# Kernel tuning notes

Measured on AMD Instinct MI355X. Metric: run time of the kernel, lower is better.

The kernel has to match this reference:

```python
import jax, jax.numpy as jnp
import numpy as np
import math

EMBED_DIM = 768
NUM_HEADS = 12
HEAD_DIM = EMBED_DIM // NUM_HEADS
R = 16
LORA_ALPHA = 16
SCALING = LORA_ALPHA / math.sqrt(R)  # 4.0
U = 1.0  # ramp_up_steps=0 -> u()=1.0


def lora_linear(x, W, b, A):
    # base F.linear + SingLoRA delta: delta_W = A @ A.T (symmetric)
    base = x @ W.T + b
    delta_W = A @ A.T  # [D, D]
    return base + (x @ delta_W.T) * (U * SCALING)


def setup_inputs() -> dict:
    key = jax.random.key(0)
    ks = jax.random.split(key, 16)
    B, S, D = 2, 2048, EMBED_DIM
    inv = 1.0 / math.sqrt(D)
    d = {
        'query': jax.random.normal(ks[0], (B, S, D), jnp.float32),
        'key': jax.random.normal(ks[1], (B, S, D), jnp.float32),
        'value': jax.random.normal(ks[2], (B, S, D), jnp.float32),
        'Wq': jax.random.normal(ks[3], (D, D), jnp.float32) * inv,
        'bq': jax.random.normal(ks[4], (D,), jnp.float32) * 0.01,
        'Aq': jax.random.normal(ks[5], (D, R), jnp.float32) * 0.01,
        'Wk': jax.random.normal(ks[6], (D, D), jnp.float32) * inv,
        'bk': jax.random.normal(ks[7], (D,), jnp.float32) * 0.01,
        'Ak': jax.random.normal(ks[8], (D, R), jnp.float32) * 0.01,
        'Wv': jax.random.normal(ks[9], (D, D), jnp.float32) * inv,
        'bv': jax.random.normal(ks[10], (D,), jnp.float32) * 0.01,
        'Av': jax.random.normal(ks[11], (D, R), jnp.float32) * 0.01,
        'Wo': jax.random.normal(ks[12], (D, D), jnp.float32) * inv,
        'bo': jax.random.normal(ks[13], (D,), jnp.float32) * 0.01,
    }
    return d


def reference(query, key, value, Wq, bq, Aq, Wk, bk, Ak, Wv, bv, Av, Wo, bo):
    B, S, D = query.shape
    H, hd = NUM_HEADS, HEAD_DIM
    q = lora_linear(query, Wq, bq, Aq)
    k = lora_linear(key, Wk, bk, Ak)
    v = lora_linear(value, Wv, bv, Av)
    # [B, S, D] -> [B, H, S, hd]
    q = q.reshape(B, S, H, hd).transpose(0, 2, 1, 3)
    k = k.reshape(B, S, H, hd).transpose(0, 2, 1, 3)
    v = v.reshape(B, S, H, hd).transpose(0, 2, 1, 3)
    scores = jnp.einsum('bhqd,bhkd->bhqk', q, k) / math.sqrt(hd)
    attn = jax.nn.softmax(scores, axis=-1)
    out = jnp.einsum('bhqk,bhkd->bhqd', attn, v)  # [B, H, S, hd]
    out = out.transpose(0, 2, 1, 3).reshape(B, S, D)
    out = out @ Wo.T + bo
    return out
```

## Files before the change

### kernel.cpp

```cpp
#include <hip/hip_runtime.h>
#include <math.h>
#include <stdint.h>

#define D 768
#define S 2048
#define B_ 2
#define NROWS 4096
#define H 12
#define HD 64
#define R_ 16

typedef _Float16 half_t;
typedef _Float16 half8 __attribute__((ext_vector_type(8)));
typedef _Float16 half4 __attribute__((ext_vector_type(4)));
typedef float floatx4 __attribute__((ext_vector_type(4)));

#define MFMA32(a, b, c) __builtin_amdgcn_mfma_f32_16x16x32_f16(a, b, c, 0, 0, 0)
#define EXP2F(x) __builtin_amdgcn_exp2f(x)

#define SWAIT(N) __builtin_amdgcn_s_waitcnt(0x0F70 | (N))
#define SBAR() __builtin_amdgcn_s_barrier()
#define SETPRIO(N) __builtin_amdgcn_s_setprio(N)

__device__ __forceinline__ void gl_lds16(const void* gp, half_t* lp) {
  __builtin_amdgcn_global_load_lds(
      (const __attribute__((address_space(1))) void*)(gp),
      (__attribute__((address_space(3))) void*)(lp), 16, 0, 0);
}


__global__ __launch_bounds__(256) void prep_kernel(
    const float* __restrict__ q, const float* __restrict__ k,
    const float* __restrict__ v, half_t* __restrict__ xq,
    half_t* __restrict__ xk, half_t* __restrict__ xv,
    const float* __restrict__ Wq, const float* __restrict__ Aq,
    const float* __restrict__ Wk, const float* __restrict__ Ak,
    const float* __restrict__ Wv, const float* __restrict__ Av,
    const float* __restrict__ Wo, half_t* __restrict__ Mq,
    half_t* __restrict__ Mk, half_t* __restrict__ Mv,
    half_t* __restrict__ Mo) {
  __shared__ float4 As[3072];
  const int bid = blockIdx.x;
  const int tid = threadIdx.x;

  if (bid < 2304) {
    const int y = bid / 768;
    const float* x = (y == 0) ? q : (y == 1) ? k : v;
    half_t* o = (y == 0) ? xq : (y == 1) ? xk : xv;
    const int base = (bid - y * 768) * 4096;
#pragma unroll
    for (int c = 0; c < 4; ++c) {
      int i = base + (tid + 256 * c) * 4;
      float4 vv = *reinterpret_cast<const float4*>(x + i);
      half_t tmp[4] = {(half_t)vv.x, (half_t)vv.y, (half_t)vv.z, (half_t)vv.w};
      *reinterpret_cast<uint64_t*>(o + i) = *reinterpret_cast<uint64_t*>(tmp);
    }
  } else if (bid < 2448) {
    const int base = (bid - 2304) * 4096;
#pragma unroll
    for (int c = 0; c < 4; ++c) {
      int i = base + (tid + 256 * c) * 4;
      float4 vv = *reinterpret_cast<const float4*>(Wo + i);
      half_t tmp[4] = {(half_t)vv.x, (half_t)vv.y, (half_t)vv.z, (half_t)vv.w};
      *reinterpret_cast<uint64_t*>(Mo + i) = *reinterpret_cast<uint64_t*>(tmp);
    }
  } else {
    const int u = bid - 2448;
    const int y = u / 192;
    const int jb = u - y * 192;
    const float* W = (y == 0) ? Wq : (y == 1) ? Wk : Wv;
    const float* A = (y == 0) ? Aq : (y == 1) ? Ak : Av;
    half_t* M = (y == 0) ? Mq : (y == 1) ? Mk : Mv;

#pragma unroll
    for (int c = 0; c < 12; ++c)
      As[tid + 256 * c] =
          *reinterpret_cast<const float4*>(A + (tid + 256 * c) * 4);
    __syncthreads();

    const int j0 = jb * 4;
    float4 aj[4][4];
#pragma unroll
    for (int jj = 0; jj < 4; ++jj)
#pragma unroll
      for (int qq = 0; qq < 4; ++qq) aj[jj][qq] = As[(j0 + jj) * 4 + qq];

#pragma unroll
    for (int c = 0; c < 3; ++c) {
      const int kk = tid + 256 * c;
      float4 ak[4];
#pragma unroll
      for (int qq = 0; qq < 4; ++qq) ak[qq] = As[kk * 4 + qq];
#pragma unroll
      for (int jj = 0; jj < 4; ++jj) {
        float s = 0.f;
#pragma unroll
        for (int qq = 0; qq < 4; ++qq)
          s += ak[qq].x * aj[jj][qq].x + ak[qq].y * aj[jj][qq].y +
               ak[qq].z * aj[jj][qq].z + ak[qq].w * aj[jj][qq].w;
        const int idx = (j0 + jj) * D + kk;
        M[idx] = (half_t)(W[idx] + 4.0f * s);
      }
    }
  }
}

__global__ __launch_bounds__(256) void gemm_qkv_kernel(
    const half_t* __restrict__ x0, const half_t* __restrict__ x1,
    const half_t* __restrict__ x2, const half_t* __restrict__ m0,
    const half_t* __restrict__ m1, const half_t* __restrict__ m2,
    const float* __restrict__ b0, const float* __restrict__ b1,
    const float* __restrict__ b2, half_t* __restrict__ o0,
    half_t* __restrict__ o1, half_t* __restrict__ o2) {
  constexpr int AG = 8;
  constexpr int G = 16;
  constexpr int PB = G * 512;
  __shared__ __align__(16) half_t smem[3 * PB];

  int lin = blockIdx.x + 6 * (blockIdx.y + 32 * blockIdx.z);
  lin = (lin & 7) * 72 + (lin >> 3);
  const int z = lin / 192;
  const int rem = lin - z * 192;
  const int by = rem / 6;
  const int bx = rem - by * 6;

  const half_t* X = (z == 0) ? x0 : (z == 1) ? x1 : x2;
  const half_t* M = (z == 0) ? m0 : (z == 1) ? m1 : m2;
  const float* bias = (z == 0) ? b0 : (z == 1) ? b1 : b2;
  half_t* Out = (z == 0) ? o0 : (z == 1) ? o1 : o2;

  const int tid = threadIdx.x;
  const int lane = tid & 63;
  const int wv = tid >> 6;
  const int lr = lane & 15;
  const int lq = lane >> 4;
  const int row0 = by * 128;
  const int j0 = bx * 128;
  const int wr = wv >> 1;
  const int wc = wv & 1;

  floatx4 acc[4][4] = {};

#define GSTAGE(soff, k0)                                                      \
  do {                                                                        \
    _Pragma("unroll") for (int gi = 0; gi < 4; ++gi) {                        \
      int g = wv * 4 + gi;                                                    \
      if (g < AG) {                                                           \
        gl_lds16(X + (size_t)(row0 + g * 16 + lr) * D + (k0) + lq * 8,        \
                 smem + (soff) + g * 512);                                    \
      } else {                                                                \
        gl_lds16(M + (size_t)(j0 + (g - AG) * 16 + lr) * D + (k0) + lq * 8,   \
                 smem + (soff) + g * 512);                                    \
      }                                                                       \
    }                                                                         \
  } while (0)

  GSTAGE(0, 0);
  GSTAGE(PB, 32);
  SWAIT(4);
  SBAR();

  int co = 0, so = 2 * PB;
  for (int it = 0; it < D / 32; ++it) {
    if (it + 2 < D / 32) GSTAGE(so, (it + 2) * 32);
    const half_t* Ab = smem + co;
    const half_t* Bb = Ab + AG * 512;
    half8 af[4], bf[4];
#pragma unroll
    for (int t = 0; t < 4; ++t)
      af[t] = *reinterpret_cast<const half8*>(
          &Ab[((wr * 4 + t) * 64 + lane) * 8]);
#pragma unroll
    for (int u = 0; u < 4; ++u)
      bf[u] = *reinterpret_cast<const half8*>(
          &Bb[((wc * 4 + u) * 64 + lane) * 8]);
#pragma unroll
    for (int t = 0; t < 4; ++t)
#pragma unroll
      for (int u = 0; u < 4; ++u) acc[t][u] = MFMA32(af[t], bf[u], acc[t][u]);
    if (it + 2 < D / 32) SWAIT(4); else SWAIT(0);
    SBAR();
    co += PB; if (co == 3 * PB) co = 0;
    so += PB; if (so == 3 * PB) so = 0;
  }
#undef GSTAGE

  float bv[4];
#pragma unroll
  for (int u = 0; u < 4; ++u) bv[u] = bias[j0 + (wc * 4 + u) * 16 + lr];

  if (z == 2) {
    const int bb = row0 >> 11;
    const int kb0 = (row0 & 2047) >> 6;
#pragma unroll
    for (int t = 0; t < 4; ++t) {
#pragma unroll
      for (int u = 0; u < 4; ++u) {
        int gc = j0 + (wc * 4 + u) * 16 + lr;
        int hh = gc >> 6;
        int ud = (gc & 63) >> 4;
        half4 hv;
#pragma unroll
        for (int r = 0; r < 4; ++r) hv[r] = (half_t)(acc[t][u][r] + bv[u]);
        size_t addr = ((size_t)(bb * H + hh) * HD) * S +
                      (size_t)(kb0 + wr) * 4096 +
                      (ud * 2 + ((t >> 1) & 1)) * 512 + lane * 8 + (t & 1) * 4;
        *reinterpret_cast<half4*>(&Out[addr]) = hv;
      }
    }
    return;
  }

#pragma unroll
  for (int t = 0; t < 4; ++t) {
#pragma unroll
    for (int u = 0; u < 4; ++u) {
#pragma unroll
      for (int r = 0; r < 4; ++r) {
        int gr = row0 + (wr * 4 + t) * 16 + lq * 4 + r;
        int gc = j0 + (wc * 4 + u) * 16 + lr;
        Out[(size_t)gr * D + gc] = (half_t)(acc[t][u][r] + bv[u]);
      }
    }
  }
}

__global__ __launch_bounds__(256) void gemm_o_kernel(
    const half_t* __restrict__ Xh, const half_t* __restrict__ M,
    const float* __restrict__ bias, float* __restrict__ Out) {
  constexpr int AG = 8;
  constexpr int G = 16;
  constexpr int PB = G * 512;
  __shared__ __align__(16) half_t smem[3 * PB];

  int lin = blockIdx.x + 12 * blockIdx.y;
  lin = (lin & 7) * 96 + (lin >> 3);
  const int bx = lin % 12;
  const int byy = lin / 12;

  const int tid = threadIdx.x;
  const int lane = tid & 63;
  const int wv = tid >> 6;
  const int lr = lane & 15;
  const int lq = lane >> 4;
  const int row0 = byy * 64;
  const int j0 = bx * 64;
  const int wr = wv >> 1;
  const int wc = wv & 1;

  floatx4 acc[2][2] = {};

#define GSTAGE(soff, k0)                                                       \
  do {                                                                         \
    _Pragma("unroll") for (int gi = 0; gi < 4; ++gi) {                         \
      int g = wv * 4 + gi;                                                     \
      if (g < AG) {                                                            \
        int t = g >> 1, c = g & 1;                                             \
        gl_lds16(                                                              \
            Xh + (size_t)(row0 + t * 16 + lr) * D + (k0) + c * 32 + lq * 8,    \
            smem + (soff) + g * 512);                                          \
      } else {                                                                 \
        int g2 = g - AG;                                                       \
        int u = g2 >> 1, c = g2 & 1;                                           \
        gl_lds16(                                                              \
            M + (size_t)(j0 + u * 16 + lr) * D + (k0) + c * 32 + lq * 8,       \
            smem + (soff) + AG * 512 + g2 * 512);                              \
      }                                                                        \
    }                                                                          \
  } while (0)

  GSTAGE(0, 0);
  GSTAGE(PB, 64);
  SWAIT(4);
  SBAR();

  int co = 0, so = 2 * PB;
  for (int it = 0; it < D / 64; ++it) {
    if (it + 2 < D / 64) GSTAGE(so, (it + 2) * 64);
    const half_t* Ab = smem + co;
    const half_t* Bb = Ab + AG * 512;
#pragma unroll
    for (int c = 0; c < 2; ++c) {
      half8 af[2], bf[2];
#pragma unroll
      for (int t = 0; t < 2; ++t)
        af[t] = *reinterpret_cast<const half8*>(
            &Ab[(((wr * 2 + t) * 2 + c) * 64 + lane) * 8]);
#pragma unroll
      for (int u = 0; u < 2; ++u)
        bf[u] = *reinterpret_cast<const half8*>(
            &Bb[(((wc * 2 + u) * 2 + c) * 64 + lane) * 8]);
#pragma unroll
      for (int t = 0; t < 2; ++t)
#pragma unroll
        for (int u = 0; u < 2; ++u) acc[t][u] = MFMA32(af[t], bf[u], acc[t][u]);
    }
    if (it + 2 < D / 64) SWAIT(4); else SWAIT(0);
    SBAR();
    co += PB; if (co == 3 * PB) co = 0;
    so += PB; if (so == 3 * PB) so = 0;
  }
#undef GSTAGE

  float bv[2];
#pragma unroll
  for (int u = 0; u < 2; ++u) bv[u] = bias[j0 + (wc * 2 + u) * 16 + lr];
#pragma unroll
  for (int t = 0; t < 2; ++t) {
#pragma unroll
    for (int u = 0; u < 2; ++u) {
#pragma unroll
      for (int r = 0; r < 4; ++r) {
        int gr = row0 + (wr * 2 + t) * 16 + lq * 4 + r;
        int gc = j0 + (wc * 2 + u) * 16 + lr;
        Out[(size_t)gr * D + gc] = acc[t][u][r] + bv[u];
      }
    }
  }
}

__global__ __launch_bounds__(256, 3) void attn_mfma_kernel(
    const half_t* __restrict__ Qh, const half_t* __restrict__ Kh,
    const half_t* __restrict__ Vt2, half_t* __restrict__ Oh) {
  __shared__ __align__(16) half_t smem[24576];
  half_t* Ks = smem;
  half_t* Vs = smem + 12288;

  const int tid = threadIdx.x;
  const int lane = tid & 63;
  const int wv = tid >> 6;
  const int qp = wv >> 1;
  const int half_ = wv & 1;
  const int lr = lane & 15;
  const int lq = lane >> 4;

  int lin = blockIdx.x + 32 * (blockIdx.y + 12 * blockIdx.z);
  lin = (lin & 7) * 96 + (lin >> 3);
  const int q0 = (lin & 31) * 64;
  const int hb = lin >> 5;
  const int h = hb % 12;
  const int b = hb / 12;

  const size_t base = (size_t)b * S * D + h * HD;
  const size_t vtbase = (size_t)(b * H + h) * HD * (size_t)S;

  const half_t qscale = (half_t)0.18033688f;
  half8 qf[2][2];
#pragma unroll
  for (int s = 0; s < 2; ++s) {
    const int qw = q0 + (qp * 2 + s) * 16;
#pragma unroll
    for (int c = 0; c < 2; ++c) {
      half8 qv = *reinterpret_cast<const half8*>(
          &Qh[base + (size_t)(qw + lr) * D + c * 32 + lq * 8]);
#pragma unroll
      for (int j = 0; j < 8; ++j) qv[j] = qv[j] * qscale;
      qf[s][c] = qv;
    }
  }

  half8 ones8;
#pragma unroll
  for (int j = 0; j < 8; ++j) ones8[j] = (half_t)1.0f;

  floatx4 o[2][4] = {};
  floatx4 ol[2] = {};

#define STAGE(soff, kb)                                                        \
  do {                                                                         \
    _Pragma("unroll") for (int gi = 0; gi < 4; ++gi) {                         \
      int g = wv * 4 + gi;                                                     \
      if (g < 8) {                                                             \
        int u = g >> 1, c = g & 1;                                             \
        gl_lds16(                                                              \
            Kh + base + (size_t)((kb) + u * 16 + lr) * D + c * 32 + lq * 8,    \
            Ks + (soff) + g * 512);                                            \
      } else {                                                                 \
        int gv = g - 8;                                                        \
        gl_lds16(Vt2 + vtbase + (size_t)(kb)*64 + gv * 512 + lane * 8,         \
                 Vs + (soff) + gv * 512);                                      \
      }                                                                        \
    }                                                                          \
  } while (0)

  STAGE(0, 0);
  STAGE(4096, 64);
  SWAIT(4);
  SBAR();

  int co = 0, so = 8192;
  for (int it = 0; it < S / 64; ++it) {
    if (it + 2 < S / 64) STAGE(so, (it + 2) * 64);

    half8 pv[2];
#pragma unroll
    for (int ui = 0; ui < 2; ++ui) {
      const int u = half_ * 2 + ui;
      half8 kf0 = *reinterpret_cast<const half8*>(
          &Ks[co + ((u * 2 + 0) * 64 + lane) * 8]);
      half8 kf1 = *reinterpret_cast<const half8*>(
          &Ks[co + ((u * 2 + 1) * 64 + lane) * 8]);
      SETPRIO(1);
      floatx4 st0 = {}, st1 = {};
      st0 = MFMA32(kf0, qf[0][0], st0);
      st0 = MFMA32(kf1, qf[0][1], st0);
      st1 = MFMA32(kf0, qf[1][0], st1);
      st1 = MFMA32(kf1, qf[1][1], st1);
      SETPRIO(0);
#pragma unroll
      for (int j = 0; j < 4; ++j) {
        pv[0][4 * ui + j] = (half_t)EXP2F(st0[j]);
        pv[1][4 * ui + j] = (half_t)EXP2F(st1[j]);
      }
    }
    SETPRIO(1);
#pragma unroll
    for (int ud = 0; ud < 4; ++ud) {
      half8 vf8 = *reinterpret_cast<const half8*>(
          &Vs[co + ((ud * 2 + half_) * 64 + lane) * 8]);
      o[0][ud] = MFMA32(pv[0], vf8, o[0][ud]);
      o[1][ud] = MFMA32(pv[1], vf8, o[1][ud]);
    }
    ol[0] = MFMA32(pv[0], ones8, ol[0]);
    ol[1] = MFMA32(pv[1], ones8, ol[1]);
    SETPRIO(0);

    if (it + 2 < S / 64) SWAIT(4); else SWAIT(0);
    SBAR();
    co += 4096; if (co == 12288) co = 0;
    so += 4096; if (so == 12288) so = 0;
  }
#undef STAGE

  float* red = (float*)smem;
  if (half_ == 1) {
#pragma unroll
    for (int s = 0; s < 2; ++s) {
      const int slot = (qp * 2 + s) * 64 + lane;
#pragma unroll
      for (int comp = 0; comp < 16; ++comp)
        red[comp * 260 + slot] = o[s][comp >> 2][comp & 3];
#pragma unroll
      for (int r = 0; r < 4; ++r) red[(16 + r) * 260 + slot] = ol[s][r];
    }
  }
  __syncthreads();
  if (half_ == 0) {
#pragma unroll
    for (int s = 0; s < 2; ++s) {
      const int slot = (qp * 2 + s) * 64 + lane;
      const int qw = q0 + (qp * 2 + s) * 16;
      float linv[4];
#pragma unroll
      for (int r = 0; r < 4; ++r)
        linv[r] = 1.0f / (ol[s][r] + red[(16 + r) * 260 + slot]);
#pragma unroll
      for (int ud = 0; ud < 4; ++ud) {
#pragma unroll
        for (int r = 0; r < 4; ++r) {
          float ov = o[s][ud][r] + red[(ud * 4 + r) * 260 + slot];
          int row = qw + lq * 4 + r;
          int col = h * HD + ud * 16 + lr;
          Oh[(size_t)(b * S + row) * D + col] = (half_t)(ov * linv[r]);
        }
      }
    }
  }
}

extern "C" void kernel_launch(void* const* d_in, const int* in_sizes, int n_in,
                              void* d_out, int out_size, void* d_ws,
                              size_t ws_size, hipStream_t stream) {
  const float* query = (const float*)d_in[0];
  const float* key   = (const float*)d_in[1];
  const float* value = (const float*)d_in[2];
  const float* Wq = (const float*)d_in[3];
  const float* bq = (const float*)d_in[4];
  const float* Aq = (const float*)d_in[5];
  const float* Wk = (const float*)d_in[6];
  const float* bk = (const float*)d_in[7];
  const float* Ak = (const float*)d_in[8];
  const float* Wv = (const float*)d_in[9];
  const float* bv = (const float*)d_in[10];
  const float* Av = (const float*)d_in[11];
  const float* Wo = (const float*)d_in[12];
  const float* bo = (const float*)d_in[13];
  float* out = (float*)d_out;

  half_t* hw = (half_t*)d_ws;
  const size_t XSZ = (size_t)NROWS * D;
  const size_t MSZ = (size_t)D * D;
  half_t* xq = hw;
  half_t* xk = xq + XSZ;
  half_t* xv = xk + XSZ;
  half_t* qh = xv + XSZ;
  half_t* kh = qh + XSZ;
  half_t* vt = kh + XSZ;
  half_t* ab = vt + XSZ;
  half_t* Mq = ab + XSZ;
  half_t* Mk = Mq + MSZ;
  half_t* Mv = Mk + MSZ;
  half_t* Mo = Mv + MSZ;

  prep_kernel<<<3024, 256, 0, stream>>>(query, key, value, xq, xk, xv, Wq, Aq,
                                        Wk, Ak, Wv, Av, Wo, Mq, Mk, Mv, Mo);

  dim3 gq(D / 128, NROWS / 128, 3);
  gemm_qkv_kernel<<<gq, 256, 0, stream>>>(xq, xk, xv, Mq, Mk, Mv, bq, bk, bv,
                                          qh, kh, vt);

  dim3 ga(S / 64, H, B_);
  attn_mfma_kernel<<<ga, 256, 0, stream>>>(qh, kh, vt, ab);

  dim3 go(D / 64, NROWS / 64, 1);
  gemm_o_kernel<<<go, 256, 0, stream>>>(ab, Mo, bo, out);
}
```

Measured before the change: 203.1 us.

## Software-pipeline attention loop to overlap next-tile QK with current exp/PV

Restructures the flash-attention inner loop into a two-stage software pipeline. The QK^T MFMAs and V-fragment LDS loads for tile t+1 are issued before the exp2 and PV MFMAs for tile t, using ping-pong register sets (A/B), with an explicit prologue and epilogue. The aim is to hide exp/transcendental latency and LDS load latency behind independent MFMA work. In exchange, register pressure rises from holding two sets of scores and V fragments, which could lower occupancy. A __syncthreads is also added before the shared-memory reduction.

```diff
diff --git a/kernel.cpp b/kernel.cpp
--- a/kernel.cpp
+++ b/kernel.cpp
@@ -383,55 +383,123 @@
     }                                                                          \
   } while (0)
 
+#define QKPHASE(v0, v1, v2, v3, s00, s01, s10, s11)                            \
+  do {                                                                         \
+    v0 = *reinterpret_cast<const half8*>(                                      \
+        &Vs[co + ((0 * 2 + half_) * 64 + lane) * 8]);                          \
+    v1 = *reinterpret_cast<const half8*>(                                      \
+        &Vs[co + ((1 * 2 + half_) * 64 + lane) * 8]);                          \
+    v2 = *reinterpret_cast<const half8*>(                                      \
+        &Vs[co + ((2 * 2 + half_) * 64 + lane) * 8]);                          \
+    v3 = *reinterpret_cast<const half8*>(                                      \
+        &Vs[co + ((3 * 2 + half_) * 64 + lane) * 8]);                          \
+    {                                                                          \
+      const int u = half_ * 2;                                                 \
+      half8 kf0 = *reinterpret_cast<const half8*>(                             \
+          &Ks[co + ((u * 2 + 0) * 64 + lane) * 8]);                            \
+      half8 kf1 = *reinterpret_cast<const half8*>(                             \
+          &Ks[co + ((u * 2 + 1) * 64 + lane) * 8]);                            \
+      SETPRIO(1);                                                              \
+      floatx4 t0 = {}, t1 = {};                                                \
+      t0 = MFMA32(kf0, qf[0][0], t0);                                          \
+      t0 = MFMA32(kf1, qf[0][1], t0);                                          \
+      t1 = MFMA32(kf0, qf[1][0], t1);                                          \
+      t1 = MFMA32(kf1, qf[1][1], t1);                                          \
+      SETPRIO(0);                                                              \
+      s00 = t0;                                                                \
+      s10 = t1;                                                                \
+    }                                                                          \
+    {                                                                          \
+      const int u = half_ * 2 + 1;                                             \
+      half8 kf0 = *reinterpret_cast<const half8*>(                             \
+          &Ks[co + ((u * 2 + 0) * 64 + lane) * 8]);                            \
+      half8 kf1 = *reinterpret_cast<const half8*>(                             \
+          &Ks[co + ((u * 2 + 1) * 64 + lane) * 8]);                            \
+      SETPRIO(1);                                                              \
+      floatx4 t0 = {}, t1 = {};                                                \
+      t0 = MFMA32(kf0, qf[0][0], t0);                                          \
+      t0 = MFMA32(kf1, qf[0][1], t0);                                          \
+      t1 = MFMA32(kf0, qf[1][0], t1);                                          \
+      t1 = MFMA32(kf1, qf[1][1], t1);                                          \
+      SETPRIO(0);                                                              \
+      s01 = t0;                                                                \
+      s11 = t1;                                                                \
+    }                                                                          \
+  } while (0)
+
+#define EXPPV(v0, v1, v2, v3, s00, s01, s10, s11)                              \
+  do {                                                                         \
+    half8 pv0, pv1;                                                            \
+    _Pragma("unroll") for (int j = 0; j < 4; ++j) {                            \
+      pv0[j] = (half_t)EXP2F(s00[j]);                                          \
+      pv0[4 + j] = (half_t)EXP2F(s01[j]);                                      \
+      pv1[j] = (half_t)EXP2F(s10[j]);                                          \
+      pv1[4 + j] = (half_t)EXP2F(s11[j]);                                      \
+    }                                                                          \
+    SETPRIO(1);                                                                \
+    o[0][0] = MFMA32(pv0, v0, o[0][0]);                                        \
+    o[1][0] = MFMA32(pv1, v0, o[1][0]);                                        \
+    o[0][1] = MFMA32(pv0, v1, o[0][1]);                                        \
+    o[1][1] = MFMA32(pv1, v1, o[1][1]);                                        \
+    o[0][2] = MFMA32(pv0, v2, o[0][2]);                                        \
+    o[1][2] = MFMA32(pv1, v2, o[1][2]);                                        \
+    o[0][3] = MFMA32(pv0, v3, o[0][3]);                                        \
+    o[1][3] = MFMA32(pv1, v3, o[1][3]);                                        \
+    ol[0] = MFMA32(pv0, ones8, ol[0]);                                         \
+    ol[1] = MFMA32(pv1, ones8, ol[1]);                                         \
+    SETPRIO(0);                                                                \
+  } while (0)
+
+#define ROT()                                                                  \
+  do {                                                                         \
+    co += 4096; if (co == 12288) co = 0;                                       \
+    so += 4096; if (so == 12288) so = 0;                                       \
+  } while (0)
+
   STAGE(0, 0);
   STAGE(4096, 64);
   SWAIT(4);
   SBAR();
 
   int co = 0, so = 8192;
-  for (int it = 0; it < S / 64; ++it) {
-    if (it + 2 < S / 64) STAGE(so, (it + 2) * 64);
-
-    half8 pv[2];
-#pragma unroll
-    for (int ui = 0; ui < 2; ++ui) {
-      const int u = half_ * 2 + ui;
-      half8 kf0 = *reinterpret_cast<const half8*>(
-          &Ks[co + ((u * 2 + 0) * 64 + lane) * 8]);
-      half8 kf1 = *reinterpret_cast<const half8*>(
-          &Ks[co + ((u * 2 + 1) * 64 + lane) * 8]);
-      SETPRIO(1);
-      floatx4 st0 = {}, st1 = {};
-      st0 = MFMA32(kf0, qf[0][0], st0);
-      st0 = MFMA32(kf1, qf[0][1], st0);
-      st1 = MFMA32(kf0, qf[1][0], st1);
-      st1 = MFMA32(kf1, qf[1][1], st1);
-      SETPRIO(0);
-#pragma unroll
-      for (int j = 0; j < 4; ++j) {
-        pv[0][4 * ui + j] = (half_t)EXP2F(st0[j]);
-        pv[1][4 * ui + j] = (half_t)EXP2F(st1[j]);
-      }
-    }
-    SETPRIO(1);
-#pragma unroll
-    for (int ud = 0; ud < 4; ++ud) {
-      half8 vf8 = *reinterpret_cast<const half8*>(
-          &Vs[co + ((ud * 2 + half_) * 64 + lane) * 8]);
-      o[0][ud] = MFMA32(pv[0], vf8, o[0][ud]);
-      o[1][ud] = MFMA32(pv[1], vf8, o[1][ud]);
-    }
-    ol[0] = MFMA32(pv[0], ones8, ol[0]);
-    ol[1] = MFMA32(pv[1], ones8, ol[1]);
-    SETPRIO(0);
-
-    if (it + 2 < S / 64) SWAIT(4); else SWAIT(0);
+  floatx4 sA00, sA01, sA10, sA11, sB00, sB01, sB10, sB11;
+  half8 vA0, vA1, vA2, vA3, vB0, vB1, vB2, vB3;
+
+  STAGE(so, 2 * 64);
+  QKPHASE(vA0, vA1, vA2, vA3, sA00, sA01, sA10, sA11);
+  SWAIT(4);
+  SBAR();
+  ROT();
+
+  for (int it = 1; it < 31; it += 2) {
+    STAGE(so, (it + 2) * 64);
+    QKPHASE(vB0, vB1, vB2, vB3, sB00, sB01, sB10, sB11);
+    EXPPV(vA0, vA1, vA2, vA3, sA00, sA01, sA10, sA11);
+    SWAIT(4);
     SBAR();
-    co += 4096; if (co == 12288) co = 0;
-    so += 4096; if (so == 12288) so = 0;
-  }
+    ROT();
+    if (it + 3 < 32) {
+      STAGE(so, (it + 3) * 64);
+      QKPHASE(vA0, vA1, vA2, vA3, sA00, sA01, sA10, sA11);
+      EXPPV(vB0, vB1, vB2, vB3, sB00, sB01, sB10, sB11);
+      SWAIT(4);
+    } else {
+      QKPHASE(vA0, vA1, vA2, vA3, sA00, sA01, sA10, sA11);
+      EXPPV(vB0, vB1, vB2, vB3, sB00, sB01, sB10, sB11);
+      SWAIT(0);
+    }
+    SBAR();
+    ROT();
+  }
+  QKPHASE(vB0, vB1, vB2, vB3, sB00, sB01, sB10, sB11);
+  EXPPV(vA0, vA1, vA2, vA3, sA00, sA01, sA10, sA11);
+  EXPPV(vB0, vB1, vB2, vB3, sB00, sB01, sB10, sB11);
 #undef STAGE
-
+#undef QKPHASE
+#undef EXPPV
+#undef ROT
+
+  __syncthreads();
   float* red = (float*)smem;
   if (half_ == 1) {
 #pragma unroll
```

New measurement: 270.8 us. 33.3% more time.
